# Kernel optimization log

Hardware: AMD Instinct MI355X
Metric: run time of the kernel (lower is better)

The kernel has to match this reference:

```python
import jax, jax.numpy as jnp
import numpy as np

S, B, D, NH = 4096, 4, 1024, 16


def _unitnorm(v):
    # v / ||v||_2 along last dim (matches torch.norm(v, dim=-1))
    return v / jnp.linalg.norm(v, axis=-1, keepdims=True)


def setup_inputs() -> dict:
    key = jax.random.key(0)
    ks = jax.random.split(key, 9)
    scale = 1.0 / np.sqrt(D)
    inp = {
        "h": jax.random.normal(ks[0], (S, B, D), dtype=jnp.float32),
        "Wq_w": jax.random.normal(ks[1], (D, D), dtype=jnp.float32) * scale,
        "Wq_b": jax.random.normal(ks[2], (D,), dtype=jnp.float32) * scale,
        "Wk_w": jax.random.normal(ks[3], (D, D), dtype=jnp.float32) * scale,
        "Wk_b": jax.random.normal(ks[4], (D,), dtype=jnp.float32) * scale,
        "Wv_w": jax.random.normal(ks[5], (D, D), dtype=jnp.float32) * scale,
        "Wv_b": jax.random.normal(ks[6], (D,), dtype=jnp.float32) * scale,
        "Wo_w": jax.random.normal(ks[7], (D, D), dtype=jnp.float32) * scale,
        "Wo_b": jax.random.normal(ks[8], (D,), dtype=jnp.float32) * scale,
        "nhead": NH,
    }
    return inp


def reference(h, Wq_w, Wq_b, Wk_w, Wk_b, Wv_w, Wv_b, Wo_w, Wo_b, nhead):
    s, b, d = h.shape
    dh = d // nhead

    def proj(W, bias):
        # torch nn.Linear: x @ W.T + b, then split heads -> [S,B,NH,dh]
        return (h @ W.T + bias).reshape(s, b, nhead, dh)

    k = jax.nn.elu(_unitnorm(proj(Wk_w, Wk_b)))  # unitelu
    v = proj(Wv_w, Wv_b)
    q = _unitnorm(proj(Wq_w, Wq_b))  # sigma = unitnorm (default)

    # Linear-attention state: sum of outer products over the whole sequence
    A = jnp.einsum('sbnq,sbnv->bnvq', k, v)  # [B,NH,dh,dh]
    out = jnp.einsum('sbnq,bnvq->sbnv', q, A).reshape(s, b, d)
    out = out @ Wo_w.T + Wo_b
    return out, k, q
```

## Files before the change

kernel.cpp:

```cpp
#include <hip/hip_runtime.h>
#include <hip/hip_bf16.h>
#include <math.h>

#define S_LEN 4096
#define B_SZ  4
#define D_DIM 1024
#define NHEAD 16
#define R_ROWS (S_LEN * B_SZ)

#define AS1 __attribute__((address_space(1)))
#define AS3 __attribute__((address_space(3)))

typedef __bf16 bf16_t;
typedef __attribute__((ext_vector_type(8))) __bf16 bf16x8;
typedef __attribute__((ext_vector_type(4))) __bf16 bf16x4;
typedef __attribute__((ext_vector_type(4))) float  f32x4;

#define MFMA16 __builtin_amdgcn_mfma_f32_16x16x32_bf16

__device__ __forceinline__ void gload16(const bf16_t* g, bf16_t* l) {
  __builtin_amdgcn_global_load_lds((const AS1 unsigned int*)g,
                                   (AS3 unsigned int*)l, 16, 0, 0);
}

#define BAR asm volatile("s_barrier" ::: "memory")
#define LGKM0 do { asm volatile("s_waitcnt lgkmcnt(0)" ::: "memory"); \
                   __builtin_amdgcn_sched_barrier(0); } while (0)

#define RD_A(dst, ap, mlo) \
  _Pragma("unroll") for (int mm = 0; mm < 4; ++mm) \
    _Pragma("unroll") for (int kx = 0; kx < 2; ++kx) \
      dst[mm][kx] = *(const bf16x8*)&ap[offA[(mlo) + mm][kx]];
#define RD_B(dst, bp, nlo) \
  _Pragma("unroll") for (int nn = 0; nn < 2; ++nn) \
    _Pragma("unroll") for (int kx = 0; kx < 2; ++kx) \
      dst[nn][kx] = *(const bf16x8*)&bp[offB[(nlo) + nn][kx]];
#define QUAD(mb, nb, AF, BF) \
  do { __builtin_amdgcn_s_setprio(1); \
  _Pragma("unroll") for (int mm = 0; mm < 4; ++mm) \
    _Pragma("unroll") for (int nn = 0; nn < 2; ++nn) { \
      acc[(mb)+mm][(nb)+nn] = MFMA16(AF[mm][0], BF[nn][0], acc[(mb)+mm][(nb)+nn], 0, 0, 0); \
      acc[(mb)+mm][(nb)+nn] = MFMA16(AF[mm][1], BF[nn][1], acc[(mb)+mm][(nb)+nn], 0, 0, 0); } \
  __builtin_amdgcn_s_setprio(0); } while (0)

__global__ void k_cvt(const float* __restrict__ src, bf16_t* __restrict__ dst, int n) {
  int i = (blockIdx.x * 256 + threadIdx.x) * 4;
  if (i >= n) return;
  f32x4 v = *(const f32x4*)(src + i);
  bf16x4 o;
  o[0] = (bf16_t)v[0]; o[1] = (bf16_t)v[1]; o[2] = (bf16_t)v[2]; o[3] = (bf16_t)v[3];
  *(bf16x4*)(dst + i) = o;
}

__device__ __forceinline__ void gemm_core_8ph(
    const bf16_t* __restrict__ A, const bf16_t* __restrict__ B,
    int row0, int col0,
    bf16_t (&sA)[2][2][8192], bf16_t (&sB)[2][2][8192], f32x4 (&acc)[8][4])
{
  const int tid  = threadIdx.x;
  const int wave = tid >> 6, lane = tid & 63;
  const int lr = lane & 15, lg = lane >> 4;
  const int wr = wave >> 2, wn = wave & 3;
  const int grow = tid >> 3;
  const int gsw  = (tid & 7) ^ (grow & 7);

  auto stA = [&](int buf, int half, int k0) {
    #pragma unroll
    for (int j = 0; j < 2; ++j)
      gload16(&A[(size_t)(row0 + half * 128 + j * 64 + grow) * D_DIM + k0 + gsw * 8],
              &sA[buf][half][(j * 64 + wave * 8) * 64]);
  };
  auto stB = [&](int buf, int half, int k0) {
    #pragma unroll
    for (int j = 0; j < 2; ++j)
      gload16(&B[(size_t)(col0 + half * 128 + j * 64 + grow) * D_DIM + k0 + gsw * 8],
              &sB[buf][half][(j * 64 + wave * 8) * 64]);
  };

  int offA[8][2], offB[4][2];
  #pragma unroll
  for (int m = 0; m < 8; ++m) {
    const int r = m * 16 + lr;
    #pragma unroll
    for (int kx = 0; kx < 2; ++kx)
      offA[m][kx] = r * 64 + (((kx << 2) + lg) ^ (r & 7)) * 8;
  }
  #pragma unroll
  for (int n = 0; n < 4; ++n) {
    const int r = (wn & 1) * 64 + n * 16 + lr;
    #pragma unroll
    for (int kx = 0; kx < 2; ++kx)
      offB[n][kx] = r * 64 + (((kx << 2) + lg) ^ (r & 7)) * 8;
  }
  const bf16_t* a0 = &sA[0][wr][0];
  const bf16_t* a1 = &sA[1][wr][0];
  const bf16_t* b0 = &sB[0][wn >> 1][0];
  const bf16_t* b1 = &sB[1][wn >> 1][0];

  #pragma unroll
  for (int m = 0; m < 8; m++)
    #pragma unroll
    for (int n = 0; n < 4; n++)
      #pragma unroll
      for (int r = 0; r < 4; r++) acc[m][n][r] = 0.f;

  stA(0, 0, 0);  stA(0, 1, 0);  stB(0, 0, 0);  stB(0, 1, 0);
  stA(1, 0, 64); stA(1, 1, 64); stB(1, 0, 64); stB(1, 1, 64);
  asm volatile("s_waitcnt vmcnt(8)" ::: "memory");
  BAR;

  bf16x8 af03[4][2], af47[4][2], bf01[2][2], bf23[2][2];

  #pragma unroll 1
  for (int i = 0; i < 8; ++i) {
    const bool last = (i == 7);
    const int kn0 = (i + 1) * 128, kn1 = kn0 + 64;

    RD_A(af03, a0, 0); RD_B(bf01, b0, 0);
    BAR; LGKM0; QUAD(0, 0, af03, bf01); BAR;
    RD_A(af47, a0, 4);
    BAR; LGKM0; QUAD(4, 0, af47, bf01); BAR;
    RD_B(bf23, b0, 2);
    if (!last) stA(0, 0, kn0);
    BAR; LGKM0; QUAD(0, 2, af03, bf23); BAR;
    if (!last) { stA(0, 1, kn0); stB(0, 0, kn0); }
    BAR; QUAD(4, 2, af47, bf23);
    if (!last) asm volatile("s_waitcnt vmcnt(6)" ::: "memory");
    else       asm volatile("s_waitcnt vmcnt(0)" ::: "memory");
    BAR;

    RD_A(af03, a1, 0); RD_B(bf01, b1, 0);
    if (!last) stB(0, 1, kn0);
    BAR; LGKM0; QUAD(0, 0, af03, bf01); BAR;
    RD_A(af47, a1, 4);
    BAR; LGKM0; QUAD(4, 0, af47, bf01); BAR;
    RD_B(bf23, b1, 2);
    if (!last) stA(1, 0, kn1);
    BAR; LGKM0; QUAD(0, 2, af03, bf23); BAR;
    if (!last) { stA(1, 1, kn1); stB(1, 0, kn1); stB(1, 1, kn1); }
    BAR; QUAD(4, 2, af47, bf23);
    if (!last) asm volatile("s_waitcnt vmcnt(8)" ::: "memory");
    BAR;
  }
}

__global__ __launch_bounds__(512, 2) void k_proj(
    const bf16_t* __restrict__ hB, const bf16_t* __restrict__ Wcat,
    const float* __restrict__ bq, const float* __restrict__ bk, const float* __restrict__ bv,
    bf16_t* __restrict__ outVb, float* __restrict__ outK, float* __restrict__ outQ,
    bf16_t* __restrict__ qBm)
{
  __shared__ bf16_t sA[2][2][8192];
  __shared__ bf16_t sB[2][2][8192];

  const int tid  = threadIdx.x;
  const int wave = tid >> 6, lane = tid & 63;
  const int lr = lane & 15, lg = lane >> 4;
  const int wr = wave >> 2, wn = wave & 3;
  const int row0 = blockIdx.x * 256;
  const int by   = blockIdx.y;

  f32x4 acc[8][4];
  gemm_core_8ph(hB, Wcat, row0, by * 256, sA, sB, acc);

  const int sec = by >> 2;
  const int hc0 = (by & 3) * 256 + wn * 64;
  const float* bias = (sec == 0) ? bq : (sec == 1 ? bk : bv);
  float bvv[4];
  #pragma unroll
  for (int n = 0; n < 4; n++) bvv[n] = bias[hc0 + n * 16 + lr];

  #pragma unroll
  for (int m = 0; m < 8; ++m) {
    #pragma unroll
    for (int r = 0; r < 4; ++r) {
      const int gm = row0 + wr * 128 + m * 16 + lg * 4 + r;
      float v[4];
      float ss = 0.f;
      #pragma unroll
      for (int n = 0; n < 4; n++) {
        v[n] = acc[m][n][r] + bvv[n];
        ss += v[n] * v[n];
      }
      if (sec == 2) {
        #pragma unroll
        for (int n = 0; n < 4; n++)
          outVb[(size_t)gm * D_DIM + hc0 + n * 16 + lr] = (bf16_t)v[n];
      } else {
        #pragma unroll
        for (int msk = 1; msk < 16; msk <<= 1) ss += __shfl_xor(ss, msk);
        const float rs = 1.0f / sqrtf(ss);
        if (sec == 0) {
          const size_t qrow = (size_t)(gm & 3) * S_LEN + (gm >> 2);
          #pragma unroll
          for (int n = 0; n < 4; n++) {
            const float qn = v[n] * rs;
            outQ[(size_t)gm * D_DIM + hc0 + n * 16 + lr] = qn;
            qBm[qrow * D_DIM + hc0 + n * 16 + lr] = (bf16_t)qn;
          }
        } else {
          #pragma unroll
          for (int n = 0; n < 4; n++) {
            float kn = v[n] * rs;
            kn = kn > 0.f ? kn : expm1f(kn);
            outK[(size_t)gm * D_DIM + hc0 + n * 16 + lr] = kn;
          }
        }
      }
    }
  }
}

__global__ __launch_bounds__(256) void k_state(
    const float* __restrict__ Kf, const bf16_t* __restrict__ Vb,
    float* __restrict__ Apart)
{
  const int bn = blockIdx.x;
  const int ch = blockIdx.y;
  const int b = bn >> 4, n = bn & 15;
  const int tid = threadIdx.x;
  const int ti = tid >> 4, tj = tid & 15;

  __shared__ float sV[32][64];
  __shared__ float sK[32][64];

  float acc[4][4];
  #pragma unroll
  for (int i = 0; i < 4; i++)
    #pragma unroll
    for (int j = 0; j < 4; j++) acc[i][j] = 0.f;

  const int rr = tid >> 3, cc = (tid & 7) * 8;
  for (int s0 = ch * 512; s0 < ch * 512 + 512; s0 += 32) {
    const size_t g = (size_t)((s0 + rr) * B_SZ + b) * D_DIM + n * 64 + cc;
    bf16x8 v8 = *(const bf16x8*)&Vb[g];
    #pragma unroll
    for (int e = 0; e < 8; e++) sV[rr][cc + e] = (float)v8[e];
    *(f32x4*)&sK[rr][cc]     = *(const f32x4*)&Kf[g];
    *(f32x4*)&sK[rr][cc + 4] = *(const f32x4*)&Kf[g + 4];
    __syncthreads();
    #pragma unroll
    for (int ss = 0; ss < 32; ss++) {
      f32x4 vv = *(const f32x4*)&sV[ss][ti * 4];
      f32x4 kk = *(const f32x4*)&sK[ss][tj * 4];
      #pragma unroll
      for (int i = 0; i < 4; i++)
        #pragma unroll
        for (int j = 0; j < 4; j++)
          acc[i][j] = fmaf(vv[i], kk[j], acc[i][j]);
    }
    __syncthreads();
  }
  float* ap = Apart + ((size_t)ch * 64 + bn) * 4096;
  #pragma unroll
  for (int i = 0; i < 4; i++)
    #pragma unroll
    for (int j = 0; j < 4; j++)
      ap[(ti * 4 + i) * 64 + tj * 4 + j] = acc[i][j];
}

__global__ __launch_bounds__(256) void k_combine(
    const float* __restrict__ Apart, const bf16_t* __restrict__ WoB,
    bf16_t* __restrict__ Ct)
{
  const int bn = blockIdx.x;
  const int dp = blockIdx.y;
  const int b = bn >> 4, n = bn & 15;
  const int tid = threadIdx.x;
  const int ti = tid >> 4, tj = tid & 15;

  __shared__ float sAm[64][65];
  __shared__ float sW[64][65];

  #pragma unroll
  for (int p = 0; p < 16; p++) {
    const int idx = tid + p * 256;
    float s = 0.f;
    #pragma unroll
    for (int c2 = 0; c2 < 8; c2++)
      s += Apart[((size_t)c2 * 64 + bn) * 4096 + idx];
    sAm[idx >> 6][idx & 63] = s;
  }
  {
    const int r = tid >> 2, cv = (tid & 3) * 16;
    bf16x8 w0 = *(const bf16x8*)&WoB[(size_t)(dp * 64 + r) * D_DIM + n * 64 + cv];
    bf16x8 w1 = *(const bf16x8*)&WoB[(size_t)(dp * 64 + r) * D_DIM + n * 64 + cv + 8];
    #pragma unroll
    for (int e = 0; e < 8; e++) {
      sW[r][cv + e]     = (float)w0[e];
      sW[r][cv + 8 + e] = (float)w1[e];
    }
  }
  __syncthreads();

  float acc[4][4];
  #pragma unroll
  for (int i = 0; i < 4; i++)
    #pragma unroll
    for (int j = 0; j < 4; j++) acc[i][j] = 0.f;

  for (int dv = 0; dv < 64; dv++) {
    float w[4], a[4];
    #pragma unroll
    for (int i = 0; i < 4; i++) w[i] = sW[ti * 4 + i][dv];
    #pragma unroll
    for (int j = 0; j < 4; j++) a[j] = sAm[dv][tj * 4 + j];
    #pragma unroll
    for (int i = 0; i < 4; i++)
      #pragma unroll
      for (int j = 0; j < 4; j++)
        acc[i][j] = fmaf(w[i], a[j], acc[i][j]);
  }
  #pragma unroll
  for (int i = 0; i < 4; i++)
    #pragma unroll
    for (int j = 0; j < 4; j++)
      Ct[((size_t)b * D_DIM + dp * 64 + ti * 4 + i) * D_DIM + n * 64 + tj * 4 + j] =
          (bf16_t)acc[i][j];
}

__global__ __launch_bounds__(512, 2) void k_final(
    const bf16_t* __restrict__ qBm, const bf16_t* __restrict__ Ct,
    const float* __restrict__ bo, float* __restrict__ outO)
{
  __shared__ bf16_t sA[2][2][8192];
  __shared__ bf16_t sB[2][2][8192];

  const int tid  = threadIdx.x;
  const int wave = tid >> 6, lane = tid & 63;
  const int lr = lane & 15, lg = lane >> 4;
  const int wr = wave >> 2, wn = wave & 3;
  const int b    = blockIdx.z;
  const int row0 = blockIdx.x * 256;
  const int col0 = blockIdx.y * 256;

  f32x4 acc[8][4];
  gemm_core_8ph(qBm + (size_t)b * S_LEN * D_DIM, Ct + (size_t)b * D_DIM * D_DIM,
                row0, col0, sA, sB, acc);

  #pragma unroll
  for (int m = 0; m < 8; ++m) {
    #pragma unroll
    for (int r = 0; r < 4; ++r) {
      const int gs = row0 + wr * 128 + m * 16 + lg * 4 + r;
      #pragma unroll
      for (int n = 0; n < 4; n++) {
        const int col = col0 + wn * 64 + n * 16 + lr;
        outO[((size_t)gs * B_SZ + b) * D_DIM + col] = acc[m][n][r] + bo[col];
      }
    }
  }
}

extern "C" void kernel_launch(void* const* d_in, const int* in_sizes, int n_in,
                              void* d_out, int out_size, void* d_ws, size_t ws_size,
                              hipStream_t stream) {
  (void)in_sizes; (void)n_in; (void)out_size; (void)ws_size;
  const float* h  = (const float*)d_in[0];
  const float* Wq = (const float*)d_in[1];
  const float* bq = (const float*)d_in[2];
  const float* Wk = (const float*)d_in[3];
  const float* bk = (const float*)d_in[4];
  const float* Wv = (const float*)d_in[5];
  const float* bv = (const float*)d_in[6];
  const float* Wo = (const float*)d_in[7];
  const float* bo = (const float*)d_in[8];

  float* out0 = (float*)d_out;
  float* outK = out0 + (size_t)R_ROWS * D_DIM;
  float* outQ = outK + (size_t)R_ROWS * D_DIM;
  bf16_t* vB  = (bf16_t*)d_out;

  char* ws = (char*)d_ws;
  bf16_t* hB    = (bf16_t*)ws;
  bf16_t* Ct    = (bf16_t*)ws;
  bf16_t* Wcat  = (bf16_t*)(ws + 33554432);
  bf16_t* WoB   = (bf16_t*)(ws + 33554432 + 6291456);
  float*  Apart = (float*)(ws + 41943040);
  bf16_t* qBm   = (bf16_t*)(ws + 50331648);

  const int nH = R_ROWS * D_DIM;
  const int nW = D_DIM * D_DIM;
  k_cvt<<<nH / 1024, 256, 0, stream>>>(h, hB, nH);
  k_cvt<<<nW / 1024, 256, 0, stream>>>(Wq, Wcat, nW);
  k_cvt<<<nW / 1024, 256, 0, stream>>>(Wk, Wcat + nW, nW);
  k_cvt<<<nW / 1024, 256, 0, stream>>>(Wv, Wcat + 2 * nW, nW);
  k_cvt<<<nW / 1024, 256, 0, stream>>>(Wo, WoB, nW);

  k_proj<<<dim3(R_ROWS / 256, 12), 512, 0, stream>>>(hB, Wcat, bq, bk, bv,
                                                     vB, outK, outQ, qBm);
  k_state<<<dim3(64, 8), 256, 0, stream>>>(outK, vB, Apart);
  k_combine<<<dim3(64, 16), 256, 0, stream>>>(Apart, WoB, Ct);
  k_final<<<dim3(S_LEN / 256, D_DIM / 256, B_SZ), 512, 0, stream>>>(qBm, Ct, bo, out0);
}
```

Baseline: 254.4 us.

## Merge weight conversions, drop redundant barriers, reorder MFMA chain in GEMM

Replaces the four separate weight fp32-to-bf16 conversion launches with a single kernel that handles all four matrices (WoB sits right after Wcat, so the contiguous write fits). Removes the leading s_barrier before each MFMA quad in the projection GEMM main loop and reorders the MFMA issue so consecutive instructions write different accumulators, avoiding back-to-back dependent accumulation. The aim is less launch overhead, fewer workgroup synchronisations and better MFMA pipelining, at the risk of LDS hazards if any removed barrier was protecting buffer reuse.

```diff
diff --git a/kernel.cpp b/kernel.cpp
--- a/kernel.cpp
+++ b/kernel.cpp
@@ -37,10 +37,10 @@
       dst[nn][kx] = *(const bf16x8*)&bp[offB[(nlo) + nn][kx]];
 #define QUAD(mb, nb, AF, BF) \
   do { __builtin_amdgcn_s_setprio(1); \
-  _Pragma("unroll") for (int mm = 0; mm < 4; ++mm) \
-    _Pragma("unroll") for (int nn = 0; nn < 2; ++nn) { \
-      acc[(mb)+mm][(nb)+nn] = MFMA16(AF[mm][0], BF[nn][0], acc[(mb)+mm][(nb)+nn], 0, 0, 0); \
-      acc[(mb)+mm][(nb)+nn] = MFMA16(AF[mm][1], BF[nn][1], acc[(mb)+mm][(nb)+nn], 0, 0, 0); } \
+  _Pragma("unroll") for (int kx = 0; kx < 2; ++kx) \
+    _Pragma("unroll") for (int mm = 0; mm < 4; ++mm) \
+      _Pragma("unroll") for (int nn = 0; nn < 2; ++nn) \
+        acc[(mb)+mm][(nb)+nn] = MFMA16(AF[mm][kx], BF[nn][kx], acc[(mb)+mm][(nb)+nn], 0, 0, 0); \
   __builtin_amdgcn_s_setprio(0); } while (0)
 
 __global__ void k_cvt(const float* __restrict__ src, bf16_t* __restrict__ dst, int n) {
@@ -50,6 +50,17 @@
   bf16x4 o;
   o[0] = (bf16_t)v[0]; o[1] = (bf16_t)v[1]; o[2] = (bf16_t)v[2]; o[3] = (bf16_t)v[3];
   *(bf16x4*)(dst + i) = o;
+}
+__global__ void k_cvtw(const float* __restrict__ q, const float* __restrict__ k,
+                       const float* __restrict__ v, const float* __restrict__ o,
+                       bf16_t* __restrict__ dst) {
+  const int sec = blockIdx.x >> 10;
+  const int i = ((blockIdx.x & 1023) * 256 + threadIdx.x) * 4;
+  const float* s = (sec == 0) ? q : (sec == 1) ? k : (sec == 2) ? v : o;
+  f32x4 x = *(const f32x4*)(s + i);
+  bf16x4 y;
+  y[0] = (bf16_t)x[0]; y[1] = (bf16_t)x[1]; y[2] = (bf16_t)x[2]; y[3] = (bf16_t)x[3];
+  *(bf16x4*)(dst + (size_t)sec * 1048576 + i) = y;
 }
 
 __device__ __forceinline__ void gemm_core_8ph(
@@ -117,28 +128,28 @@
     const int kn0 = (i + 1) * 128, kn1 = kn0 + 64;
 
     RD_A(af03, a0, 0); RD_B(bf01, b0, 0);
-    BAR; LGKM0; QUAD(0, 0, af03, bf01); BAR;
+    LGKM0; QUAD(0, 0, af03, bf01); BAR;
     RD_A(af47, a0, 4);
-    BAR; LGKM0; QUAD(4, 0, af47, bf01); BAR;
+    LGKM0; QUAD(4, 0, af47, bf01); BAR;
     RD_B(bf23, b0, 2);
     if (!last) stA(0, 0, kn0);
-    BAR; LGKM0; QUAD(0, 2, af03, bf23); BAR;
+    LGKM0; QUAD(0, 2, af03, bf23); BAR;
     if (!last) { stA(0, 1, kn0); stB(0, 0, kn0); }
-    BAR; QUAD(4, 2, af47, bf23);
+    QUAD(4, 2, af47, bf23);
     if (!last) asm volatile("s_waitcnt vmcnt(6)" ::: "memory");
     else       asm volatile("s_waitcnt vmcnt(0)" ::: "memory");
     BAR;
 
     RD_A(af03, a1, 0); RD_B(bf01, b1, 0);
     if (!last) stB(0, 1, kn0);
-    BAR; LGKM0; QUAD(0, 0, af03, bf01); BAR;
+    LGKM0; QUAD(0, 0, af03, bf01); BAR;
     RD_A(af47, a1, 4);
-    BAR; LGKM0; QUAD(4, 0, af47, bf01); BAR;
+    LGKM0; QUAD(4, 0, af47, bf01); BAR;
     RD_B(bf23, b1, 2);
     if (!last) stA(1, 0, kn1);
-    BAR; LGKM0; QUAD(0, 2, af03, bf23); BAR;
+    LGKM0; QUAD(0, 2, af03, bf23); BAR;
     if (!last) { stA(1, 1, kn1); stB(1, 0, kn1); stB(1, 1, kn1); }
-    BAR; QUAD(4, 2, af47, bf23);
+    QUAD(4, 2, af47, bf23);
     if (!last) asm volatile("s_waitcnt vmcnt(8)" ::: "memory");
     BAR;
   }
@@ -380,15 +391,11 @@
   bf16_t* qBm   = (bf16_t*)(ws + 50331648);
 
   const int nH = R_ROWS * D_DIM;
-  const int nW = D_DIM * D_DIM;
   k_cvt<<<nH / 1024, 256, 0, stream>>>(h, hB, nH);
-  k_cvt<<<nW / 1024, 256, 0, stream>>>(Wq, Wcat, nW);
-  k_cvt<<<nW / 1024, 256, 0, stream>>>(Wk, Wcat + nW, nW);
-  k_cvt<<<nW / 1024, 256, 0, stream>>>(Wv, Wcat + 2 * nW, nW);
-  k_cvt<<<nW / 1024, 256, 0, stream>>>(Wo, WoB, nW);
-
-  k_proj<<<dim3(R_ROWS / 256, 12), 512, 0, stream>>>(hB, Wcat, bq, bk, bv,
-                                                     vB, outK, outQ, qBm);
+  k_cvtw<<<4096, 256, 0, stream>>>(Wq, Wk, Wv, Wo, Wcat);
+
+  k_proj<<<dim3(64, 12), 512, 0, stream>>>(hB, Wcat, bq, bk, bv,
+                                           vB, outK, outQ, qBm);
   k_state<<<dim3(64, 8), 256, 0, stream>>>(outK, vB, Apart);
   k_combine<<<dim3(64, 16), 256, 0, stream>>>(Apart, WoB, Ct);
   k_final<<<dim3(S_LEN / 256, D_DIM / 256, B_SZ), 512, 0, stream>>>(qBm, Ct, bo, out0);
```

Result: faster. 243.5 us (median of 2 runs) (-4.3%).
